# Optimization experiments

Measured on AMD Instinct MI355X. Metric: run time of the kernel, lower is better.

The kernel has to match this reference:

```python
import jax, jax.numpy as jnp
import numpy as np

N_EMBED = 1024
NUM_HEADS = 16
HEAD_DIM = N_EMBED // NUM_HEADS

def setup_inputs() -> dict:
    key = jax.random.key(0)
    ks = jax.random.split(key, 7)
    s = 0.02
    return {
        "x": jax.random.normal(ks[0], (2, 2048, N_EMBED), dtype=jnp.float32),
        "Wqkv": jax.random.normal(ks[1], (N_EMBED, 3 * N_EMBED), dtype=jnp.float32) * s,
        "bqkv": jax.random.normal(ks[2], (3 * N_EMBED,), dtype=jnp.float32) * s,
        "W1": jax.random.normal(ks[3], (N_EMBED, 4 * N_EMBED), dtype=jnp.float32) * s,
        "b1": jax.random.normal(ks[4], (4 * N_EMBED,), dtype=jnp.float32) * s,
        "W2": jax.random.normal(ks[5], (4 * N_EMBED, N_EMBED), dtype=jnp.float32) * s,
        "b2": jax.random.normal(ks[6], (N_EMBED,), dtype=jnp.float32) * s,
    }

def reference(x, Wqkv, bqkv, W1, b1, W2, b2):
    B, T, N = x.shape
    h, n = NUM_HEADS, HEAD_DIM
    # LayerNorm in source is identity; dropout=0 (eval)
    qkv = x @ Wqkv + bqkv  # [B,T,3N]
    q, k, v = jnp.split(qkv, 3, axis=-1)
    q = q.reshape(B, T, h, n).transpose(0, 2, 1, 3)  # [B,h,T,n]
    k = k.reshape(B, T, h, n).transpose(0, 2, 1, 3)
    v = v.reshape(B, T, h, n).transpose(0, 2, 1, 3)
    scores = jnp.einsum('bhqd,bhkd->bhqk', q, k) / jnp.sqrt(jnp.float32(n))
    causal = jnp.tril(jnp.ones((T, T), dtype=bool))
    scores = jnp.where(causal, scores, -jnp.inf)
    attn = jax.nn.softmax(scores, axis=-1)
    out = jnp.einsum('bhqk,bhkd->bhqd', attn, v)
    out = out.transpose(0, 2, 1, 3).reshape(B, T, N)
    x = x + out  # residual (no output projection in source)
    # MLP
    hcore = jax.nn.relu(x @ W1 + b1)
    x = x + (hcore @ W2 + b2)
    return x
```

## Files before the change

kernel.cpp:

```cpp
#include <hip/hip_runtime.h>

#define NEMB 1024
#define NH 16
#define HD 64
#define TT 2048
#define BTOT 4096

typedef unsigned short u16;
typedef __bf16 bf16_t;
typedef bf16_t bf16x8 __attribute__((ext_vector_type(8)));
typedef float f32x4 __attribute__((ext_vector_type(4)));
typedef u16 u16x4 __attribute__((ext_vector_type(4)));

typedef const __attribute__((address_space(1))) void* gvp;
typedef __attribute__((address_space(3))) void* lvp;

static __device__ __forceinline__ u16 f2bf(float f) {
  unsigned u = __builtin_bit_cast(unsigned, f);
  u += 0x7fffu + ((u >> 16) & 1u);
  return (u16)(u >> 16);
}

__global__ void cvt_bf16_k(const float* __restrict__ in, u16* __restrict__ out, int n4) {
  int i = blockIdx.x * blockDim.x + threadIdx.x;
  if (i >= n4) return;
  float4 f = ((const float4*)in)[i];
  u16x4 o = { f2bf(f.x), f2bf(f.y), f2bf(f.z), f2bf(f.w) };
  ((u16x4*)out)[i] = o;
}

__global__ void transpose_cvt_k(const float* __restrict__ in, u16* __restrict__ out, int R, int C) {
  __shared__ float tile[32][33];
  int bx = blockIdx.x, by = blockIdx.y;
  int tx = threadIdx.x, ty = threadIdx.y;
  #pragma unroll
  for (int j = 0; j < 32; j += 8)
    tile[ty + j][tx] = in[(size_t)(by * 32 + ty + j) * C + bx * 32 + tx];
  __syncthreads();
  #pragma unroll
  for (int j = 0; j < 32; j += 8)
    out[(size_t)(bx * 32 + ty + j) * R + by * 32 + tx] = f2bf(tile[tx][ty + j]);
}

template<int EPI>
__global__ void gemm_bt(const u16* __restrict__ A, const u16* __restrict__ Bt,
                        const float* __restrict__ bias, int M, int N, int K,
                        const float* __restrict__ res, float* __restrict__ outf,
                        u16* __restrict__ o0, u16* __restrict__ o1, u16* __restrict__ o2)
{
  __shared__ u16 As[128 * 32];
  __shared__ u16 Bs[128 * 32];
  const int tid = threadIdx.x;
  const int wave = tid >> 6, lane = tid & 63;
  const int l16 = lane & 15, lq = lane >> 4;
  const int row0 = blockIdx.x * 128, col0 = blockIdx.y * 128;
  const int wm = (wave >> 1) * 64, wn = (wave & 1) * 64;
  f32x4 acc[4][4] = {};

  for (int k0 = 0; k0 < K; k0 += 32) {
    #pragma unroll
    for (int c = 0; c < 2; ++c) {
      int li = c * 256 + wave * 64 + lane;
      const u16* ga = A  + (size_t)(row0 + (li >> 2)) * K + k0 + (li & 3) * 8;
      const u16* gb = Bt + (size_t)(col0 + (li >> 2)) * K + k0 + (li & 3) * 8;
      __builtin_amdgcn_global_load_lds((gvp)ga, (lvp)&As[(c * 256 + wave * 64) * 8], 16, 0, 0);
      __builtin_amdgcn_global_load_lds((gvp)gb, (lvp)&Bs[(c * 256 + wave * 64) * 8], 16, 0, 0);
    }
    __syncthreads();
    bf16x8 af[4], bfr[4];
    #pragma unroll
    for (int i = 0; i < 4; ++i) af[i]  = *(const bf16x8*)&As[(wm + i * 16 + l16) * 32 + lq * 8];
    #pragma unroll
    for (int j = 0; j < 4; ++j) bfr[j] = *(const bf16x8*)&Bs[(wn + j * 16 + l16) * 32 + lq * 8];
    #pragma unroll
    for (int i = 0; i < 4; ++i)
      #pragma unroll
      for (int j = 0; j < 4; ++j)
        acc[i][j] = __builtin_amdgcn_mfma_f32_16x16x32_bf16(af[i], bfr[j], acc[i][j], 0, 0, 0);
    __syncthreads();
  }

  #pragma unroll
  for (int i = 0; i < 4; ++i)
    #pragma unroll
    for (int j = 0; j < 4; ++j)
      #pragma unroll
      for (int r = 0; r < 4; ++r) {
        int grow = row0 + wm + i * 16 + lq * 4 + r;
        int gcol = col0 + wn + j * 16 + l16;
        float v = acc[i][j][r] + bias[gcol];
        if constexpr (EPI == 0) {
          int b = grow >> 11, t = grow & 2047;
          int sec = gcol >> 10, rem = gcol & 1023;
          int h = rem >> 6, d = rem & 63;
          u16 bits = f2bf(v);
          size_t bh = (size_t)(b * NH + h);
          if (sec == 0)      o0[(bh * TT + t) * HD + d] = bits;
          else if (sec == 1) o1[(bh * TT + t) * HD + d] = bits;
          else               o2[(bh * HD + d) * TT + t] = bits;
        } else if constexpr (EPI == 1) {
          v = fmaxf(v, 0.f);
          o0[(size_t)grow * N + gcol] = f2bf(v);
        } else {
          size_t idx = (size_t)grow * N + gcol;
          outf[idx] = v + res[idx];
        }
      }
}

__global__ void __launch_bounds__(256, 4)
attn_k(const u16* __restrict__ qb, const u16* __restrict__ kb,
       const u16* __restrict__ vtb, const float* __restrict__ x,
       float* __restrict__ xres, u16* __restrict__ xresbf)
{
  __shared__ u16 P[4][16 * 72];
  const int id = blockIdx.x;
  const int xcd = id & 7, r8 = id >> 3;
  const int bh = xcd * 4 + (r8 >> 5);
  const int xq = 31 - (r8 & 31);
  const int b = bh >> 4, h = bh & 15;
  const int tid = threadIdx.x, wave = tid >> 6, lane = tid & 63;
  const int l16 = lane & 15, lq = lane >> 4;
  const u16* qh = qb + (size_t)bh * TT * HD;
  const u16* kh = kb + (size_t)bh * TT * HD;
  const u16* vh = vtb + (size_t)bh * HD * TT;
  const int q0 = (xq * 4 + wave) * 16;

  bf16x8 qf[2];
  #pragma unroll
  for (int kd = 0; kd < 2; ++kd)
    qf[kd] = *(const bf16x8*)&qh[(q0 + l16) * HD + kd * 32 + lq * 8];

  f32x4 oacc[4] = {};
  float mrow = -1e30f, lrow = 0.f;
  const int qg = q0 + l16;

  const int nkv = (q0 >> 6) + 1;
  u16* Pw = P[wave];

  for (int kv = 0; kv < nkv; ++kv) {
    const int kv0 = kv * 64;
    const bool diag = (kv0 + 63 > q0);

    bf16x8 kf[8];
    #pragma unroll
    for (int n = 0; n < 4; ++n)
      #pragma unroll
      for (int kd = 0; kd < 2; ++kd)
        kf[n * 2 + kd] = *(const bf16x8*)&kh[(kv0 + n * 16 + l16) * HD + kd * 32 + lq * 8];
    f32x4 sacc[4] = {};
    #pragma unroll
    for (int n = 0; n < 4; ++n)
      #pragma unroll
      for (int kd = 0; kd < 2; ++kd)
        sacc[n] = __builtin_amdgcn_mfma_f32_16x16x32_bf16(kf[n * 2 + kd], qf[kd], sacc[n], 0, 0, 0);

    bf16x8 vf0[4];
    #pragma unroll
    for (int nd = 0; nd < 4; ++nd)
      vf0[nd] = *(const bf16x8*)&vh[(nd * 16 + l16) * TT + kv0 + lq * 8];

    float smax = -1e30f;
    #pragma unroll
    for (int n = 0; n < 4; ++n)
      #pragma unroll
      for (int r = 0; r < 4; ++r) {
        float s = sacc[n][r] * 0.125f;
        if (diag && (kv0 + n * 16 + lq * 4 + r) > qg) s = -1e30f;
        sacc[n][r] = s;
        smax = fmaxf(smax, s);
      }
    smax = fmaxf(smax, __shfl_xor(smax, 16, 64));
    smax = fmaxf(smax, __shfl_xor(smax, 32, 64));
    const float mnew = fmaxf(mrow, smax);
    const float scl = __expf(mrow - mnew);
    float rsum = 0.f;
    #pragma unroll
    for (int n = 0; n < 4; ++n)
      #pragma unroll
      for (int r = 0; r < 4; ++r) {
        float p = __expf(sacc[n][r] - mnew);
        sacc[n][r] = p;
        rsum += p;
      }
    rsum += __shfl_xor(rsum, 16, 64);
    rsum += __shfl_xor(rsum, 32, 64);
    mrow = mnew;
    lrow = lrow * scl + rsum;

    float sclr[4];
    #pragma unroll
    for (int r = 0; r < 4; ++r) sclr[r] = __shfl(scl, lq * 4 + r, 64);
    #pragma unroll
    for (int nd = 0; nd < 4; ++nd)
      #pragma unroll
      for (int r = 0; r < 4; ++r) oacc[nd][r] *= sclr[r];

    #pragma unroll
    for (int n = 0; n < 4; ++n)
      #pragma unroll
      for (int i = 0; i < 2; ++i) {
        unsigned pk = (unsigned)f2bf(sacc[n][2 * i]) | ((unsigned)f2bf(sacc[n][2 * i + 1]) << 16);
        *(unsigned*)&Pw[l16 * 72 + n * 16 + lq * 4 + 2 * i] = pk;
      }

    bf16x8 vf1[4];
    #pragma unroll
    for (int nd = 0; nd < 4; ++nd)
      vf1[nd] = *(const bf16x8*)&vh[(nd * 16 + l16) * TT + kv0 + 32 + lq * 8];

    bf16x8 pf0 = *(const bf16x8*)&Pw[l16 * 72 + lq * 8];
    #pragma unroll
    for (int nd = 0; nd < 4; ++nd)
      oacc[nd] = __builtin_amdgcn_mfma_f32_16x16x32_bf16(pf0, vf0[nd], oacc[nd], 0, 0, 0);
    bf16x8 pf1 = *(const bf16x8*)&Pw[l16 * 72 + 32 + lq * 8];
    #pragma unroll
    for (int nd = 0; nd < 4; ++nd)
      oacc[nd] = __builtin_amdgcn_mfma_f32_16x16x32_bf16(pf1, vf1[nd], oacc[nd], 0, 0, 0);
  }

  float invr[4];
  #pragma unroll
  for (int r = 0; r < 4; ++r) invr[r] = 1.f / __shfl(lrow, lq * 4 + r, 64);
  #pragma unroll
  for (int r = 0; r < 4; ++r) {
    const int t = q0 + lq * 4 + r;
    const size_t rowbase = ((size_t)b * TT + t) * NEMB + h * HD;
    #pragma unroll
    for (int nd = 0; nd < 4; ++nd) {
      size_t idx = rowbase + nd * 16 + l16;
      float v = oacc[nd][r] * invr[r] + x[idx];
      xres[idx] = v;
      xresbf[idx] = f2bf(v);
    }
  }
}

extern "C" void kernel_launch(void* const* d_in, const int* in_sizes, int n_in,
                              void* d_out, int out_size, void* d_ws, size_t ws_size,
                              hipStream_t stream) {
  const float* x    = (const float*)d_in[0];
  const float* Wqkv = (const float*)d_in[1];
  const float* bqkv = (const float*)d_in[2];
  const float* W1   = (const float*)d_in[3];
  const float* b1   = (const float*)d_in[4];
  const float* W2   = (const float*)d_in[5];
  const float* b2   = (const float*)d_in[6];
  float* out = (float*)d_out;

  char* ws = (char*)d_ws;
  u16* x_bf   = (u16*)(ws);
  u16* wqkvt  = (u16*)(ws + 8388608);
  u16* w1t    = (u16*)(ws + 14680064);
  u16* w2t    = (u16*)(ws + 23068672);
  u16* qbuf   = (u16*)(ws + 31457280);
  u16* kbuf   = (u16*)(ws + 39845888);
  u16* vtbuf  = (u16*)(ws + 48234496);
  float* xres = (float*)(ws + 56623104);
  u16* xresbf = (u16*)(ws + 73400320);
  u16* hbuf   = (u16*)(ws + 81788928);

  cvt_bf16_k<<<4096, 256, 0, stream>>>(x, x_bf, 1048576);
  transpose_cvt_k<<<dim3(96, 32),  dim3(32, 8), 0, stream>>>(Wqkv, wqkvt, 1024, 3072);
  transpose_cvt_k<<<dim3(128, 32), dim3(32, 8), 0, stream>>>(W1, w1t, 1024, 4096);
  transpose_cvt_k<<<dim3(32, 128), dim3(32, 8), 0, stream>>>(W2, w2t, 4096, 1024);

  gemm_bt<0><<<dim3(32, 24), 256, 0, stream>>>(x_bf, wqkvt, bqkv, BTOT, 3 * NEMB, NEMB,
                                               nullptr, nullptr, qbuf, kbuf, vtbuf);
  attn_k<<<1024, 256, 0, stream>>>(qbuf, kbuf, vtbuf, x, xres, xresbf);
  gemm_bt<1><<<dim3(32, 32), 256, 0, stream>>>(xresbf, w1t, b1, BTOT, 4 * NEMB, NEMB,
                                               nullptr, nullptr, hbuf, nullptr, nullptr);
  gemm_bt<2><<<dim3(32, 8), 256, 0, stream>>>(hbuf, w2t, b2, BTOT, NEMB, 4 * NEMB,
                                              xres, out, nullptr, nullptr, nullptr);
}
```

Baseline: 492.2 us.

## Double-buffer K loads in attention and balance causal work across heads

Result: faster. 422.4 us (-14.2%).

```diff
diff --git a/kernel.cpp b/kernel.cpp
--- a/kernel.cpp
+++ b/kernel.cpp
@@ -108,7 +108,7 @@
       }
 }
 
-__global__ void __launch_bounds__(256, 4)
+__global__ void __launch_bounds__(256, 2)
 attn_k(const u16* __restrict__ qb, const u16* __restrict__ kb,
        const u16* __restrict__ vtb, const float* __restrict__ x,
        float* __restrict__ xres, u16* __restrict__ xresbf)
@@ -116,8 +116,13 @@
   __shared__ u16 P[4][16 * 72];
   const int id = blockIdx.x;
   const int xcd = id & 7, r8 = id >> 3;
-  const int bh = xcd * 4 + (r8 >> 5);
-  const int xq = 31 - (r8 & 31);
+  const int hslot = r8 >> 5, c = r8 & 31;
+  const int bh = xcd * 4 + hslot;
+  int xq;
+  if      (hslot == 0) xq = 31 - c;
+  else if (hslot == 1) xq = c;
+  else if (hslot == 2) xq = (47 - c) & 31;
+  else                 xq = (c + 16) & 31;
   const int b = bh >> 4, h = bh & 15;
   const int tid = threadIdx.x, wave = tid >> 6, lane = tid & 63;
   const int l16 = lane & 15, lq = lane >> 4;
@@ -138,16 +143,16 @@
   const int nkv = (q0 >> 6) + 1;
   u16* Pw = P[wave];
 
-  for (int kv = 0; kv < nkv; ++kv) {
-    const int kv0 = kv * 64;
-    const bool diag = (kv0 + 63 > q0);
-
-    bf16x8 kf[8];
+  auto loadk = [&](bf16x8 (&kf)[8], int kv0) {
     #pragma unroll
     for (int n = 0; n < 4; ++n)
       #pragma unroll
       for (int kd = 0; kd < 2; ++kd)
         kf[n * 2 + kd] = *(const bf16x8*)&kh[(kv0 + n * 16 + l16) * HD + kd * 32 + lq * 8];
+  };
+
+  auto body = [&](const bf16x8 (&kf)[8], int kv0) {
+    const bool diag = (kv0 + 63 > q0);
     f32x4 sacc[4] = {};
     #pragma unroll
     for (int n = 0; n < 4; ++n)
@@ -155,10 +160,12 @@
       for (int kd = 0; kd < 2; ++kd)
         sacc[n] = __builtin_amdgcn_mfma_f32_16x16x32_bf16(kf[n * 2 + kd], qf[kd], sacc[n], 0, 0, 0);
 
-    bf16x8 vf0[4];
-    #pragma unroll
-    for (int nd = 0; nd < 4; ++nd)
-      vf0[nd] = *(const bf16x8*)&vh[(nd * 16 + l16) * TT + kv0 + lq * 8];
+    bf16x8 vf[8];
+    #pragma unroll
+    for (int nd = 0; nd < 4; ++nd) {
+      vf[nd]     = *(const bf16x8*)&vh[(nd * 16 + l16) * TT + kv0 + lq * 8];
+      vf[4 + nd] = *(const bf16x8*)&vh[(nd * 16 + l16) * TT + kv0 + 32 + lq * 8];
+    }
 
     float smax = -1e30f;
     #pragma unroll
@@ -204,19 +211,25 @@
         *(unsigned*)&Pw[l16 * 72 + n * 16 + lq * 4 + 2 * i] = pk;
       }
 
-    bf16x8 vf1[4];
+    bf16x8 pf0 = *(const bf16x8*)&Pw[l16 * 72 + lq * 8];
     #pragma unroll
     for (int nd = 0; nd < 4; ++nd)
-      vf1[nd] = *(const bf16x8*)&vh[(nd * 16 + l16) * TT + kv0 + 32 + lq * 8];
-
-    bf16x8 pf0 = *(const bf16x8*)&Pw[l16 * 72 + lq * 8];
+      oacc[nd] = __builtin_amdgcn_mfma_f32_16x16x32_bf16(pf0, vf[nd], oacc[nd], 0, 0, 0);
+    bf16x8 pf1 = *(const bf16x8*)&Pw[l16 * 72 + 32 + lq * 8];
     #pragma unroll
     for (int nd = 0; nd < 4; ++nd)
-      oacc[nd] = __builtin_amdgcn_mfma_f32_16x16x32_bf16(pf0, vf0[nd], oacc[nd], 0, 0, 0);
-    bf16x8 pf1 = *(const bf16x8*)&Pw[l16 * 72 + 32 + lq * 8];
-    #pragma unroll
-    for (int nd = 0; nd < 4; ++nd)
-      oacc[nd] = __builtin_amdgcn_mfma_f32_16x16x32_bf16(pf1, vf1[nd], oacc[nd], 0, 0, 0);
+      oacc[nd] = __builtin_amdgcn_mfma_f32_16x16x32_bf16(pf1, vf[4 + nd], oacc[nd], 0, 0, 0);
+  };
+
+  bf16x8 kfA[8], kfB[8];
+  loadk(kfA, 0);
+  for (int kv = 0; kv < nkv; ) {
+    if (kv + 1 < nkv) loadk(kfB, (kv + 1) * 64);
+    body(kfA, kv * 64);
+    ++kv; if (kv == nkv) break;
+    if (kv + 1 < nkv) loadk(kfA, (kv + 1) * 64);
+    body(kfB, kv * 64);
+    ++kv;
   }
 
   float invr[4];
```
